# Kernel optimization log

Measured on AMD Instinct MI355X. Metric: run time of the kernel, lower is better.

The kernel has to match this reference:

```python
import jax, jax.numpy as jnp
import numpy as np

S, B, D, F, E, K = 1024, 2, 512, 2048, 8, 2


def setup_inputs() -> dict:
    key = jax.random.key(0)
    ks = jax.random.split(key, 12)
    s = lambda *sh: 1.0 / np.sqrt(sh[0])
    inp = {
        "x": jax.random.normal(ks[0], (S, B, D), dtype=jnp.float32),
        # gate: nn.Linear(d_model, n_experts)
        "Wg": jax.random.normal(ks[1], (D, E), dtype=jnp.float32) * s(D),
        "bg": jnp.zeros((E,), dtype=jnp.float32),
        # routed experts: stacked FFN params (E copies of expert)
        "W1": jax.random.normal(ks[2], (E, D, F), dtype=jnp.float32) * s(D),
        "b1": jnp.zeros((E, F), dtype=jnp.float32),
        "W2": jax.random.normal(ks[3], (E, F, D), dtype=jnp.float32) * s(F),
        "b2": jnp.zeros((E, D), dtype=jnp.float32),
        # shared expert (single FFN)
        "Ws1": jax.random.normal(ks[4], (D, F), dtype=jnp.float32) * s(D),
        "bs1": jnp.zeros((F,), dtype=jnp.float32),
        "Ws2": jax.random.normal(ks[5], (F, D), dtype=jnp.float32) * s(F),
        "bs2": jnp.zeros((D,), dtype=jnp.float32),
    }
    return inp


def reference(x, Wg, bg, W1, b1, W2, b2, Ws1, bs1, Ws2, bs2):
    # gate_logits: (S, B, E)
    gate_logits = jnp.einsum("sbd,de->sbe", x, Wg) + bg
    # top-k per token (eval mode: k = n_experts_per_token, t = 1.0)
    weights, selected = jax.lax.top_k(gate_logits, K)  # (S,B,K)
    weights = jax.nn.softmax(weights.astype(jnp.float32), axis=-1)
    # combine weights per expert: (S,B,E)
    onehot = jax.nn.one_hot(selected, E, dtype=weights.dtype)  # (S,B,K,E)
    comb = jnp.einsum("sbk,sbke->sbe", weights, onehot)
    # routed experts computed densely, combined with per-token routing weight
    h = jax.nn.relu(jnp.einsum("sbd,edf->sbef", x, W1) + b1)  # (S,B,E,F)
    y = jnp.einsum("sbef,efd->sbed", h, W2) + b2              # (S,B,E,D)
    out = jnp.einsum("sbe,sbed->sbd", comb, y)
    # shared expert, scaled by 1/k
    hs = jax.nn.relu(jnp.einsum("sbd,df->sbf", x, Ws1) + bs1)
    shared = jnp.einsum("sbf,fd->sbd", hs, Ws2) + bs2
    out = out + (1.0 / K) * shared
    return out
```

## Files before the change

kernel.cpp:

```cpp
#include <hip/hip_runtime.h>
#include <hip/hip_bf16.h>
#include <stdint.h>

#define TT 2048
#define DD 512
#define FF 2048
#define EE 8

typedef unsigned short u16;
typedef __attribute__((ext_vector_type(8))) unsigned short ushort8v;
typedef __attribute__((ext_vector_type(8))) short short8;
typedef __attribute__((ext_vector_type(4))) float float4v;

__device__ __forceinline__ u16 f2bf(float f) {
    unsigned u = __float_as_uint(f);
    u += 0x7FFF + ((u >> 16) & 1);
    return (u16)(u >> 16);
}

__device__ __forceinline__ void gl_lds16(const u16* g, u16* l) {
    __builtin_amdgcn_global_load_lds(
        (const __attribute__((address_space(1))) unsigned int*)g,
        (__attribute__((address_space(3))) unsigned int*)l, 16, 0, 0);
}

#define WS_HB   0ull
#define WS_XG   (WS_HB + 6144ull*2048*2)
#define WS_WT   (WS_XG + 2048ull*512*2)
#define WS_RTG  (WS_WT + 9ull*2048*512*2)
#define WS_ME   (WS_RTG + 64)
#define WS_MW   (WS_ME + 4096*4)
#define WS_RT   (WS_MW + 4096*4)
#define WS_WROW (WS_RT + 4096*4)

__global__ __launch_bounds__(256) void conv_k(const float* __restrict__ srcE,
                                              const float* __restrict__ srcS,
                                              u16* __restrict__ dst,
                                              int R, int C, int shC) {
    int mid = blockIdx.x >> 8;
    int t2  = blockIdx.x & 255;
    int tr = t2 >> shC, tc = t2 & ((1 << shC) - 1);
    int r0 = tr * 64, c0 = tc * 64;
    const float* src = (mid < 8) ? srcE + (size_t)mid * R * C : srcS;
    u16* dstm = dst + (size_t)mid * R * C;
    int t = threadIdx.x;
    __shared__ __align__(16) u16 Ls[64 * 72];
#pragma unroll
    for (int i = 0; i < 4; ++i) {
        int rr = (t >> 4) + i * 16;
        int cc = (t & 15) * 4;
        float4v v = *(const float4v*)(src + (size_t)(r0 + rr) * C + c0 + cc);
#pragma unroll
        for (int j = 0; j < 4; ++j) Ls[(cc + j) * 72 + rr] = f2bf(v[j]);
    }
    __syncthreads();
#pragma unroll
    for (int jj = 0; jj < 2; ++jj) {
        int slot = t + jj * 256;
        int cc = slot >> 3;
        int r8 = (slot & 7) * 8;
        ushort8v o = *(const ushort8v*)&Ls[cc * 72 + r8];
        *(ushort8v*)(dstm + (size_t)(c0 + cc) * R + r0 + r8) = o;
    }
}

__global__ void gate_k(const float* __restrict__ x, const float* __restrict__ Wg,
                       const float* __restrict__ bg,
                       int* __restrict__ metaE, float* __restrict__ metaW,
                       u16* __restrict__ xg) {
    int t = blockIdx.x;
    int lane = threadIdx.x;
    const float* xp = x + (size_t)t * DD + lane * 8;
    float4v x0 = *(const float4v*)xp;
    float4v x1 = *(const float4v*)(xp + 4);
    float xf[8] = {x0[0], x0[1], x0[2], x0[3], x1[0], x1[1], x1[2], x1[3]};
    float acc[EE] = {0.f, 0.f, 0.f, 0.f, 0.f, 0.f, 0.f, 0.f};
#pragma unroll
    for (int g = 0; g < 8; ++g) {
        int d = lane * 8 + g;
        const float* wp = Wg + (size_t)d * EE;
        float4v w0 = *(const float4v*)wp;
        float4v w1 = *(const float4v*)(wp + 4);
        acc[0] += xf[g] * w0[0]; acc[1] += xf[g] * w0[1];
        acc[2] += xf[g] * w0[2]; acc[3] += xf[g] * w0[3];
        acc[4] += xf[g] * w1[0]; acc[5] += xf[g] * w1[1];
        acc[6] += xf[g] * w1[2]; acc[7] += xf[g] * w1[3];
    }
#pragma unroll
    for (int off = 1; off < 64; off <<= 1) {
#pragma unroll
        for (int e = 0; e < EE; ++e) acc[e] += __shfl_xor(acc[e], off, 64);
    }
    ushort8v xv;
#pragma unroll
    for (int j = 0; j < 4; ++j) xv[j] = f2bf(x0[j]);
#pragma unroll
    for (int j = 0; j < 4; ++j) xv[4 + j] = f2bf(x1[j]);
    *(ushort8v*)(xg + (size_t)t * DD + lane * 8) = xv;
    if (lane == 0) {
#pragma unroll
        for (int e = 0; e < EE; ++e) acc[e] += bg[e];
        int e0 = 0; float l0 = acc[0];
#pragma unroll
        for (int e = 1; e < EE; ++e) if (acc[e] > l0) { l0 = acc[e]; e0 = e; }
        int e1 = -1; float l1 = -3.4e38f;
#pragma unroll
        for (int e = 0; e < EE; ++e)
            if (e != e0 && acc[e] > l1) { l1 = acc[e]; e1 = e; }
        float ex = __expf(l1 - l0);
        float w0 = 1.f / (1.f + ex);
        float w1 = 1.f - w0;
        metaE[2 * t] = e0; metaE[2 * t + 1] = e1;
        metaW[2 * t] = w0; metaW[2 * t + 1] = w1;
    }
}

__global__ __launch_bounds__(1024) void rank_k(const int* __restrict__ metaE,
                                               const float* __restrict__ metaW,
                                               int* __restrict__ routing,
                                               int* __restrict__ rtok,
                                               float* __restrict__ wrow) {
    int tid = threadIdx.x;
    int wv = tid >> 6, lane = tid & 63;
    __shared__ int segCnt[64][8];
    __shared__ int segBase[64][8];
    __shared__ int expOff[8];
    int myE[4], myRk[4];
    unsigned long long below = (lane == 0) ? 0ull : ((~0ull) >> (64 - lane));
#pragma unroll
    for (int r = 0; r < 4; ++r) {
        int entry = wv * 256 + r * 64 + lane;
        int e = metaE[entry];
        myE[r] = e;
        int rk = 0;
#pragma unroll
        for (int ee = 0; ee < 8; ++ee) {
            unsigned long long m = __ballot(e == ee);
            if (e == ee) rk = __popcll(m & below);
            if (lane == ee) segCnt[wv * 4 + r][ee] = __popcll(m);
        }
        myRk[r] = rk;
    }
    __syncthreads();
    if (tid < 8) {
        int s = 0;
        for (int g = 0; g < 64; ++g) { segBase[g][tid] = s; s += segCnt[g][tid]; }
        expOff[tid] = s;
    }
    __syncthreads();
    if (tid == 0) {
        int s = 0;
        for (int e = 0; e < 8; ++e) { int c = expOff[e]; expOff[e] = s; s += c; }
    }
    __syncthreads();
    if (tid < 8) {
        routing[tid] = expOff[tid];
        routing[8 + tid] = segBase[63][tid] + segCnt[63][tid];
    }
#pragma unroll
    for (int r = 0; r < 4; ++r) {
        int entry = wv * 256 + r * 64 + lane;
        int e = myE[r];
        int row = expOff[e] + segBase[wv * 4 + r][e] + myRk[r];
        rtok[row] = entry >> 1;
        wrow[row] = metaW[entry];
    }
}

__global__ __launch_bounds__(256) void gemmA_k(
    const u16* __restrict__ xg, const u16* __restrict__ Wt,
    const float* __restrict__ b1, const float* __restrict__ bs1,
    const int* __restrict__ routing, const int* __restrict__ rtok,
    u16* __restrict__ hbuf) {
    const int* offs = routing;
    const int* cnt = routing + 8;
    int vb = blockIdx.x;
    int tid = threadIdx.x;
    int rt, ct, Mloc, hRowBase, rowBase;
    bool routed;
    const u16* Bsrc;
    const float* bias;
    if (vb < 2048) {
        int e = vb & 7;
        int r2 = vb >> 3;
        rt = r2 >> 4; ct = r2 & 15;
        int M = cnt[e];
        if (rt * 128 >= M) return;
        Mloc = M - rt * 128;
        rowBase = offs[e] + rt * 128;
        Bsrc = Wt + (size_t)e * FF * DD;
        bias = b1 + e * FF;
        hRowBase = rowBase;
        routed = true;
    } else {
        int v = vb - 2048;
        rt = v >> 4; ct = v & 15;
        Mloc = 128;
        rowBase = rt * 128;
        Bsrc = Wt + (size_t)8 * FF * DD;
        bias = bs1;
        hRowBase = 4096 + rt * 128;
        routed = false;
    }
    int n0 = ct * 128;
    int lane = tid & 63, w = tid >> 6, ln = lane & 15, quad = lane >> 4;
    int rowL = lane >> 2;
    int kcL = (lane & 3) * 8;

    const u16* Abase[2];
#pragma unroll
    for (int i = 0; i < 2; ++i) {
        int seg = w * 2 + i;
        int rr = seg * 16 + rowL;
        int tok;
        if (routed) {
            int br = rowBase + rr;
            if (br > 4095) br = 4095;
            tok = rtok[br];
        } else {
            tok = rowBase + rr;
        }
        Abase[i] = xg + (size_t)tok * DD + kcL;
    }

    __shared__ __align__(16) u16 As[128 * 32];
    __shared__ __align__(16) u16 Bs[128 * 32];

    float4v acc[4][4];
#pragma unroll
    for (int a = 0; a < 4; ++a)
#pragma unroll
        for (int b = 0; b < 4; ++b) acc[a][b] = (float4v){0.f, 0.f, 0.f, 0.f};

    for (int kt = 0; kt < DD / 32; ++kt) {
        int k0 = kt * 32;
#pragma unroll
        for (int i = 0; i < 2; ++i) {
            int seg = w * 2 + i;
            int row = seg * 16 + rowL;
            gl_lds16(Abase[i] + k0, &As[seg * 512]);
            gl_lds16(Bsrc + (size_t)(n0 + row) * DD + k0 + kcL, &Bs[seg * 512]);
        }
        __syncthreads();
        short8 Af[4], Bf[4];
#pragma unroll
        for (int a = 0; a < 4; ++a)
            Af[a] = *(const short8*)&As[((w & 1) * 64 + a * 16 + ln) * 32 + quad * 8];
#pragma unroll
        for (int b = 0; b < 4; ++b)
            Bf[b] = *(const short8*)&Bs[((w >> 1) * 64 + b * 16 + ln) * 32 + quad * 8];
#pragma unroll
        for (int a = 0; a < 4; ++a)
#pragma unroll
            for (int b = 0; b < 4; ++b)
                acc[a][b] = __builtin_amdgcn_mfma_f32_16x16x32_bf16(Af[a], Bf[b], acc[a][b], 0, 0, 0);
        __syncthreads();
    }
#pragma unroll
    for (int b = 0; b < 4; ++b) {
        int n = n0 + (w >> 1) * 64 + b * 16 + ln;
        float bv = bias[n];
#pragma unroll
        for (int a = 0; a < 4; ++a) {
#pragma unroll
            for (int i = 0; i < 4; ++i) {
                int lr = (w & 1) * 64 + a * 16 + quad * 4 + i;
                if (lr < Mloc) {
                    float v = acc[a][b][i] + bv;
                    v = v > 0.f ? v : 0.f;
                    hbuf[(size_t)(hRowBase + lr) * FF + n] = f2bf(v);
                }
            }
        }
    }
}

__global__ __launch_bounds__(256) void gemmB_k(
    const u16* __restrict__ hbuf, const u16* __restrict__ Wt,
    const float* __restrict__ b2, const float* __restrict__ bs2,
    const int* __restrict__ routing, const int* __restrict__ rtok,
    const float* __restrict__ wrow, float* __restrict__ out) {
    const int* offs = routing;
    const int* cnt = routing + 8;
    int vb = blockIdx.x;
    int tid = threadIdx.x;
    int rt, ct, ks, Mloc, aRowBase;
    bool sh = vb >= 1024;
    const u16* Bsrc;
    const float* bias;
    if (!sh) {
        int e = vb & 7;
        int r2 = vb >> 3;
        rt = r2 >> 3; ct = (r2 >> 1) & 3; ks = r2 & 1;
        int M = cnt[e];
        if (rt * 128 >= M) return;
        Mloc = M - rt * 128;
        aRowBase = offs[e] + rt * 128;
        Bsrc = Wt + (size_t)e * DD * FF;
        bias = b2 + e * DD;
    } else {
        int v = vb - 1024;
        rt = v >> 3; ct = (v >> 1) & 3; ks = v & 1;
        Mloc = 128;
        aRowBase = 4096 + rt * 128;
        Bsrc = Wt + (size_t)8 * DD * FF;
        bias = bs2;
    }
    int n0 = ct * 128;
    int lane = tid & 63, w = tid >> 6, ln = lane & 15, quad = lane >> 4;
    int rowL = lane >> 2;
    int kcL = (lane & 3) * 8;

    __shared__ __align__(16) u16 As[128 * 32];
    __shared__ __align__(16) u16 Bs[128 * 32];

    float4v acc[4][4];
#pragma unroll
    for (int a = 0; a < 4; ++a)
#pragma unroll
        for (int b = 0; b < 4; ++b) acc[a][b] = (float4v){0.f, 0.f, 0.f, 0.f};

    const u16* Asrc = hbuf + (size_t)aRowBase * FF;

    for (int kt = 0; kt < 32; ++kt) {
        int k0 = ks * 1024 + kt * 32;
#pragma unroll
        for (int i = 0; i < 2; ++i) {
            int seg = w * 2 + i;
            int row = seg * 16 + rowL;
            gl_lds16(Asrc + (size_t)row * FF + k0 + kcL, &As[seg * 512]);
            gl_lds16(Bsrc + (size_t)(n0 + row) * FF + k0 + kcL, &Bs[seg * 512]);
        }
        __syncthreads();
        short8 Af[4], Bf[4];
#pragma unroll
        for (int a = 0; a < 4; ++a)
            Af[a] = *(const short8*)&As[((w & 1) * 64 + a * 16 + ln) * 32 + quad * 8];
#pragma unroll
        for (int b = 0; b < 4; ++b)
            Bf[b] = *(const short8*)&Bs[((w >> 1) * 64 + b * 16 + ln) * 32 + quad * 8];
#pragma unroll
        for (int a = 0; a < 4; ++a)
#pragma unroll
            for (int b = 0; b < 4; ++b)
                acc[a][b] = __builtin_amdgcn_mfma_f32_16x16x32_bf16(Af[a], Bf[b], acc[a][b], 0, 0, 0);
        __syncthreads();
    }
    float bv[4];
#pragma unroll
    for (int b = 0; b < 4; ++b)
        bv[b] = (ks == 0) ? bias[n0 + (w >> 1) * 64 + b * 16 + ln] : 0.f;
#pragma unroll
    for (int a = 0; a < 4; ++a) {
#pragma unroll
        for (int i = 0; i < 4; ++i) {
            int lr = (w & 1) * 64 + a * 16 + quad * 4 + i;
            if (lr < Mloc) {
                int row = aRowBase + lr;
                int t; float wr;
                if (sh) { t = row - 4096; wr = 0.5f; }
                else    { t = rtok[row];  wr = wrow[row]; }
                float* op = out + (size_t)t * DD;
#pragma unroll
                for (int b = 0; b < 4; ++b) {
                    int n = n0 + (w >> 1) * 64 + b * 16 + ln;
                    atomicAdd(op + n, wr * (acc[a][b][i] + bv[b]));
                }
            }
        }
    }
}

extern "C" void kernel_launch(void* const* d_in, const int* in_sizes, int n_in,
                              void* d_out, int out_size, void* d_ws, size_t ws_size,
                              hipStream_t stream) {
    const float* x   = (const float*)d_in[0];
    const float* Wg  = (const float*)d_in[1];
    const float* bg  = (const float*)d_in[2];
    const float* W1  = (const float*)d_in[3];
    const float* b1  = (const float*)d_in[4];
    const float* W2  = (const float*)d_in[5];
    const float* b2  = (const float*)d_in[6];
    const float* Ws1 = (const float*)d_in[7];
    const float* bs1 = (const float*)d_in[8];
    const float* Ws2 = (const float*)d_in[9];
    const float* bs2 = (const float*)d_in[10];
    float* out = (float*)d_out;

    char* ws = (char*)d_ws;
    u16*   hbuf    = (u16*)(ws + WS_HB);
    u16*   xg      = (u16*)(ws + WS_XG);
    u16*   Wt      = (u16*)(ws + WS_WT);
    int*   routing = (int*)(ws + WS_RTG);
    int*   metaE   = (int*)(ws + WS_ME);
    float* metaW   = (float*)(ws + WS_MW);
    int*   rtok    = (int*)(ws + WS_RT);
    float* wrow    = (float*)(ws + WS_WROW);

    hipMemsetAsync(d_out, 0, (size_t)out_size * sizeof(float), stream);

    conv_k<<<2304, 256, 0, stream>>>(W1, Ws1, Wt, DD, FF, 5);
    gate_k<<<TT, 64, 0, stream>>>(x, Wg, bg, metaE, metaW, xg);
    rank_k<<<1, 1024, 0, stream>>>(metaE, metaW, routing, rtok, wrow);
    gemmA_k<<<2304, 256, 0, stream>>>(xg, Wt, b1, bs1, routing, rtok, hbuf);
    conv_k<<<2304, 256, 0, stream>>>(W2, Ws2, Wt, FF, DD, 3);
    gemmB_k<<<1152, 256, 0, stream>>>(hbuf, Wt, b2, bs2, routing, rtok, wrow, out);
}
```

Measured before the change: 228.9 us.

## Fuse all MoE stages into one cooperative persistent kernel with grid syncs

Replaces the six separate launches plus memset with a single cooperative persistent kernel that loops over job lists, separated by grid-wide barriers. It also adds an XOR swizzle to LDS staging in both GEMMs to cut bank conflicts, raises gemmB's K-split from 2 to 4, and reorders jobs so shared-expert tiles come first. The aim is to remove launch gaps and tail effects. The cost is grid-sync overhead, a single-block rank phase that idles the rest of the GPU, and possible occupancy limits from the forced 4-blocks-per-SM bound.

```diff
diff --git a/kernel.cpp b/kernel.cpp
--- a/kernel.cpp
+++ b/kernel.cpp
@@ -1,11 +1,15 @@
 #include <hip/hip_runtime.h>
+#include <hip/hip_cooperative_groups.h>
 #include <hip/hip_bf16.h>
 #include <stdint.h>
+
+namespace cg = cooperative_groups;
 
 #define TT 2048
 #define DD 512
 #define FF 2048
 #define EE 8
+#define NJOB 2304
 
 typedef unsigned short u16;
 typedef __attribute__((ext_vector_type(8))) unsigned short ushort8v;
@@ -33,52 +37,50 @@
 #define WS_RT   (WS_MW + 4096*4)
 #define WS_WROW (WS_RT + 4096*4)
 
-__global__ __launch_bounds__(256) void conv_k(const float* __restrict__ srcE,
-                                              const float* __restrict__ srcS,
-                                              u16* __restrict__ dst,
-                                              int R, int C, int shC) {
-    int mid = blockIdx.x >> 8;
-    int t2  = blockIdx.x & 255;
+struct Params {
+    const float *x, *Wg, *bg, *W1, *b1, *W2, *b2, *Ws1, *bs1, *Ws2, *bs2;
+    float* out;
+    u16 *hbuf, *xg, *Wt;
+    int* routing; int* metaE; float* metaW; int* rtok; float* wrow;
+};
+
+__device__ void conv_unit(int j, const float* __restrict__ srcE,
+                          const float* __restrict__ srcS, u16* __restrict__ dst,
+                          int R, int C, int shC, u16* Ls) {
+    int mid = j >> 8, t2 = j & 255;
     int tr = t2 >> shC, tc = t2 & ((1 << shC) - 1);
     int r0 = tr * 64, c0 = tc * 64;
     const float* src = (mid < 8) ? srcE + (size_t)mid * R * C : srcS;
     u16* dstm = dst + (size_t)mid * R * C;
     int t = threadIdx.x;
-    __shared__ __align__(16) u16 Ls[64 * 72];
 #pragma unroll
     for (int i = 0; i < 4; ++i) {
         int rr = (t >> 4) + i * 16;
         int cc = (t & 15) * 4;
         float4v v = *(const float4v*)(src + (size_t)(r0 + rr) * C + c0 + cc);
 #pragma unroll
-        for (int j = 0; j < 4; ++j) Ls[(cc + j) * 72 + rr] = f2bf(v[j]);
+        for (int jx = 0; jx < 4; ++jx) Ls[(cc + jx) * 72 + rr] = f2bf(v[jx]);
     }
     __syncthreads();
 #pragma unroll
     for (int jj = 0; jj < 2; ++jj) {
         int slot = t + jj * 256;
-        int cc = slot >> 3;
-        int r8 = (slot & 7) * 8;
+        int cc = slot >> 3, r8 = (slot & 7) * 8;
         ushort8v o = *(const ushort8v*)&Ls[cc * 72 + r8];
         *(ushort8v*)(dstm + (size_t)(c0 + cc) * R + r0 + r8) = o;
     }
-}
-
-__global__ void gate_k(const float* __restrict__ x, const float* __restrict__ Wg,
-                       const float* __restrict__ bg,
-                       int* __restrict__ metaE, float* __restrict__ metaW,
-                       u16* __restrict__ xg) {
-    int t = blockIdx.x;
-    int lane = threadIdx.x;
-    const float* xp = x + (size_t)t * DD + lane * 8;
+    __syncthreads();
+}
+
+__device__ void gate_wave(int t, int lane, const Params& p) {
+    const float* xp = p.x + (size_t)t * DD + lane * 8;
     float4v x0 = *(const float4v*)xp;
     float4v x1 = *(const float4v*)(xp + 4);
     float xf[8] = {x0[0], x0[1], x0[2], x0[3], x1[0], x1[1], x1[2], x1[3]};
     float acc[EE] = {0.f, 0.f, 0.f, 0.f, 0.f, 0.f, 0.f, 0.f};
 #pragma unroll
     for (int g = 0; g < 8; ++g) {
-        int d = lane * 8 + g;
-        const float* wp = Wg + (size_t)d * EE;
+        const float* wp = p.Wg + (size_t)(lane * 8 + g) * EE;
         float4v w0 = *(const float4v*)wp;
         float4v w1 = *(const float4v*)(wp + 4);
         acc[0] += xf[g] * w0[0]; acc[1] += xf[g] * w0[1];
@@ -93,13 +95,13 @@
     }
     ushort8v xv;
 #pragma unroll
-    for (int j = 0; j < 4; ++j) xv[j] = f2bf(x0[j]);
-#pragma unroll
-    for (int j = 0; j < 4; ++j) xv[4 + j] = f2bf(x1[j]);
-    *(ushort8v*)(xg + (size_t)t * DD + lane * 8) = xv;
+    for (int jx = 0; jx < 4; ++jx) xv[jx] = f2bf(x0[jx]);
+#pragma unroll
+    for (int jx = 0; jx < 4; ++jx) xv[4 + jx] = f2bf(x1[jx]);
+    *(ushort8v*)(p.xg + (size_t)t * DD + lane * 8) = xv;
     if (lane == 0) {
 #pragma unroll
-        for (int e = 0; e < EE; ++e) acc[e] += bg[e];
+        for (int e = 0; e < EE; ++e) acc[e] += p.bg[e];
         int e0 = 0; float l0 = acc[0];
 #pragma unroll
         for (int e = 1; e < EE; ++e) if (acc[e] > l0) { l0 = acc[e]; e0 = e; }
@@ -109,129 +111,91 @@
             if (e != e0 && acc[e] > l1) { l1 = acc[e]; e1 = e; }
         float ex = __expf(l1 - l0);
         float w0 = 1.f / (1.f + ex);
-        float w1 = 1.f - w0;
-        metaE[2 * t] = e0; metaE[2 * t + 1] = e1;
-        metaW[2 * t] = w0; metaW[2 * t + 1] = w1;
-    }
-}
-
-__global__ __launch_bounds__(1024) void rank_k(const int* __restrict__ metaE,
-                                               const float* __restrict__ metaW,
-                                               int* __restrict__ routing,
-                                               int* __restrict__ rtok,
-                                               float* __restrict__ wrow) {
-    int tid = threadIdx.x;
-    int wv = tid >> 6, lane = tid & 63;
-    __shared__ int segCnt[64][8];
-    __shared__ int segBase[64][8];
-    __shared__ int expOff[8];
-    int myE[4], myRk[4];
+        p.metaE[2 * t] = e0; p.metaE[2 * t + 1] = e1;
+        p.metaW[2 * t] = w0; p.metaW[2 * t + 1] = 1.f - w0;
+    }
+}
+
+__device__ void rank_block(const Params& p, char* smem) {
+    u16* er      = (u16*)smem;
+    int* segCnt  = (int*)(smem + 8192);
+    int* segBase = (int*)(smem + 10240);
+    int* expTot  = (int*)(smem + 12288);
+    int tid = threadIdx.x, wv = tid >> 6, lane = tid & 63;
     unsigned long long below = (lane == 0) ? 0ull : ((~0ull) >> (64 - lane));
-#pragma unroll
-    for (int r = 0; r < 4; ++r) {
-        int entry = wv * 256 + r * 64 + lane;
-        int e = metaE[entry];
-        myE[r] = e;
+    for (int s = wv * 16; s < wv * 16 + 16; ++s) {
+        int entry = s * 64 + lane;
+        int e = p.metaE[entry];
         int rk = 0;
 #pragma unroll
         for (int ee = 0; ee < 8; ++ee) {
             unsigned long long m = __ballot(e == ee);
             if (e == ee) rk = __popcll(m & below);
-            if (lane == ee) segCnt[wv * 4 + r][ee] = __popcll(m);
-        }
-        myRk[r] = rk;
+            if (lane == ee) segCnt[s * 8 + ee] = __popcll(m);
+        }
+        er[entry] = (u16)(e | (rk << 4));
     }
     __syncthreads();
     if (tid < 8) {
         int s = 0;
-        for (int g = 0; g < 64; ++g) { segBase[g][tid] = s; s += segCnt[g][tid]; }
-        expOff[tid] = s;
+        for (int g = 0; g < 64; ++g) { segBase[g * 8 + tid] = s; s += segCnt[g * 8 + tid]; }
+        expTot[tid] = s;
     }
     __syncthreads();
     if (tid == 0) {
         int s = 0;
-        for (int e = 0; e < 8; ++e) { int c = expOff[e]; expOff[e] = s; s += c; }
-    }
-    __syncthreads();
-    if (tid < 8) {
-        routing[tid] = expOff[tid];
-        routing[8 + tid] = segBase[63][tid] + segCnt[63][tid];
-    }
-#pragma unroll
-    for (int r = 0; r < 4; ++r) {
-        int entry = wv * 256 + r * 64 + lane;
-        int e = myE[r];
-        int row = expOff[e] + segBase[wv * 4 + r][e] + myRk[r];
-        rtok[row] = entry >> 1;
-        wrow[row] = metaW[entry];
-    }
-}
-
-__global__ __launch_bounds__(256) void gemmA_k(
-    const u16* __restrict__ xg, const u16* __restrict__ Wt,
-    const float* __restrict__ b1, const float* __restrict__ bs1,
-    const int* __restrict__ routing, const int* __restrict__ rtok,
-    u16* __restrict__ hbuf) {
-    const int* offs = routing;
-    const int* cnt = routing + 8;
-    int vb = blockIdx.x;
+        for (int e = 0; e < 8; ++e) { int c = expTot[e]; expTot[8 + e] = s; s += c; }
+    }
+    __syncthreads();
+    if (tid < 8) { p.routing[tid] = expTot[8 + tid]; p.routing[8 + tid] = expTot[tid]; }
+    for (int i = 0; i < 16; ++i) {
+        int entry = tid + i * 256;
+        int v = er[entry];
+        int e = v & 15, rk = v >> 4;
+        int row = expTot[8 + e] + segBase[(entry >> 6) * 8 + e] + rk;
+        p.rtok[row] = entry >> 1;
+        p.wrow[row] = p.metaW[entry];
+    }
+    __syncthreads();
+}
+
+__device__ void gemmA_job(int j, const Params& p, u16* As, u16* Bs) {
+    const int* offs = p.routing; const int* cnt = p.routing + 8;
     int tid = threadIdx.x;
-    int rt, ct, Mloc, hRowBase, rowBase;
-    bool routed;
-    const u16* Bsrc;
-    const float* bias;
-    if (vb < 2048) {
-        int e = vb & 7;
-        int r2 = vb >> 3;
-        rt = r2 >> 4; ct = r2 & 15;
-        int M = cnt[e];
-        if (rt * 128 >= M) return;
-        Mloc = M - rt * 128;
-        rowBase = offs[e] + rt * 128;
-        Bsrc = Wt + (size_t)e * FF * DD;
-        bias = b1 + e * FF;
-        hRowBase = rowBase;
-        routed = true;
+    int rt, ct, Mloc, hRowBase, rowBase; bool routed;
+    const u16* Bsrc; const float* bias;
+    if (j < 256) {
+        rt = j >> 4; ct = j & 15; Mloc = 128; rowBase = rt * 128;
+        Bsrc = p.Wt + (size_t)8 * FF * DD; bias = p.bs1;
+        hRowBase = 4096 + rt * 128; routed = false;
     } else {
-        int v = vb - 2048;
-        rt = v >> 4; ct = v & 15;
-        Mloc = 128;
-        rowBase = rt * 128;
-        Bsrc = Wt + (size_t)8 * FF * DD;
-        bias = bs1;
-        hRowBase = 4096 + rt * 128;
-        routed = false;
+        int jr = j - 256; rt = jr >> 7; int rem = jr & 127;
+        int e = rem >> 4; ct = rem & 15;
+        int M = cnt[e]; if (rt * 128 >= M) return;
+        Mloc = M - rt * 128; rowBase = offs[e] + rt * 128;
+        Bsrc = p.Wt + (size_t)e * FF * DD; bias = p.b1 + e * FF;
+        hRowBase = rowBase; routed = true;
     }
     int n0 = ct * 128;
     int lane = tid & 63, w = tid >> 6, ln = lane & 15, quad = lane >> 4;
     int rowL = lane >> 2;
-    int kcL = (lane & 3) * 8;
-
+    int kS = ((lane & 3) ^ ((lane >> 3) & 3)) * 8;
     const u16* Abase[2];
 #pragma unroll
     for (int i = 0; i < 2; ++i) {
-        int seg = w * 2 + i;
-        int rr = seg * 16 + rowL;
+        int rr = (w * 2 + i) * 16 + rowL;
         int tok;
         if (routed) {
-            int br = rowBase + rr;
-            if (br > 4095) br = 4095;
-            tok = rtok[br];
-        } else {
-            tok = rowBase + rr;
-        }
-        Abase[i] = xg + (size_t)tok * DD + kcL;
-    }
-
-    __shared__ __align__(16) u16 As[128 * 32];
-    __shared__ __align__(16) u16 Bs[128 * 32];
-
+            int br = rowBase + rr; if (br > 4095) br = 4095;
+            tok = p.rtok[br];
+        } else tok = rowBase + rr;
+        Abase[i] = p.xg + (size_t)tok * DD + kS;
+    }
     float4v acc[4][4];
 #pragma unroll
     for (int a = 0; a < 4; ++a)
 #pragma unroll
         for (int b = 0; b < 4; ++b) acc[a][b] = (float4v){0.f, 0.f, 0.f, 0.f};
-
     for (int kt = 0; kt < DD / 32; ++kt) {
         int k0 = kt * 32;
 #pragma unroll
@@ -239,16 +203,17 @@
             int seg = w * 2 + i;
             int row = seg * 16 + rowL;
             gl_lds16(Abase[i] + k0, &As[seg * 512]);
-            gl_lds16(Bsrc + (size_t)(n0 + row) * DD + k0 + kcL, &Bs[seg * 512]);
+            gl_lds16(Bsrc + (size_t)(n0 + row) * DD + k0 + kS, &Bs[seg * 512]);
         }
         __syncthreads();
+        int rsw = (ln >> 1) & 3;
         short8 Af[4], Bf[4];
 #pragma unroll
         for (int a = 0; a < 4; ++a)
-            Af[a] = *(const short8*)&As[((w & 1) * 64 + a * 16 + ln) * 32 + quad * 8];
+            Af[a] = *(const short8*)&As[((w & 1) * 64 + a * 16 + ln) * 32 + ((quad ^ rsw) * 8)];
 #pragma unroll
         for (int b = 0; b < 4; ++b)
-            Bf[b] = *(const short8*)&Bs[((w >> 1) * 64 + b * 16 + ln) * 32 + quad * 8];
+            Bf[b] = *(const short8*)&Bs[((w >> 1) * 64 + b * 16 + ln) * 32 + ((quad ^ rsw) * 8)];
 #pragma unroll
         for (int a = 0; a < 4; ++a)
 #pragma unroll
@@ -268,77 +233,57 @@
                 if (lr < Mloc) {
                     float v = acc[a][b][i] + bv;
                     v = v > 0.f ? v : 0.f;
-                    hbuf[(size_t)(hRowBase + lr) * FF + n] = f2bf(v);
+                    p.hbuf[(size_t)(hRowBase + lr) * FF + n] = f2bf(v);
                 }
             }
         }
     }
 }
 
-__global__ __launch_bounds__(256) void gemmB_k(
-    const u16* __restrict__ hbuf, const u16* __restrict__ Wt,
-    const float* __restrict__ b2, const float* __restrict__ bs2,
-    const int* __restrict__ routing, const int* __restrict__ rtok,
-    const float* __restrict__ wrow, float* __restrict__ out) {
-    const int* offs = routing;
-    const int* cnt = routing + 8;
-    int vb = blockIdx.x;
+__device__ void gemmB_job(int j, const Params& p, u16* As, u16* Bs) {
+    const int* offs = p.routing; const int* cnt = p.routing + 8;
     int tid = threadIdx.x;
-    int rt, ct, ks, Mloc, aRowBase;
-    bool sh = vb >= 1024;
-    const u16* Bsrc;
-    const float* bias;
-    if (!sh) {
-        int e = vb & 7;
-        int r2 = vb >> 3;
-        rt = r2 >> 3; ct = (r2 >> 1) & 3; ks = r2 & 1;
-        int M = cnt[e];
-        if (rt * 128 >= M) return;
-        Mloc = M - rt * 128;
-        aRowBase = offs[e] + rt * 128;
-        Bsrc = Wt + (size_t)e * DD * FF;
-        bias = b2 + e * DD;
+    int rt, ct, ks, Mloc, aRowBase; bool sh;
+    const u16* Bsrc; const float* bias;
+    if (j < 256) {
+        sh = true; rt = j >> 4; int sub = j & 15; ct = sub >> 2; ks = sub & 3;
+        Mloc = 128; aRowBase = 4096 + rt * 128;
+        Bsrc = p.Wt + (size_t)8 * DD * FF; bias = p.bs2;
     } else {
-        int v = vb - 1024;
-        rt = v >> 3; ct = (v >> 1) & 3; ks = v & 1;
-        Mloc = 128;
-        aRowBase = 4096 + rt * 128;
-        Bsrc = Wt + (size_t)8 * DD * FF;
-        bias = bs2;
+        sh = false; int jr = j - 256; rt = jr >> 7; int rem = jr & 127;
+        int e = rem >> 4; int sub = rem & 15; ct = sub >> 2; ks = sub & 3;
+        int M = cnt[e]; if (rt * 128 >= M) return;
+        Mloc = M - rt * 128; aRowBase = offs[e] + rt * 128;
+        Bsrc = p.Wt + (size_t)e * DD * FF; bias = p.b2 + e * DD;
     }
     int n0 = ct * 128;
     int lane = tid & 63, w = tid >> 6, ln = lane & 15, quad = lane >> 4;
     int rowL = lane >> 2;
-    int kcL = (lane & 3) * 8;
-
-    __shared__ __align__(16) u16 As[128 * 32];
-    __shared__ __align__(16) u16 Bs[128 * 32];
-
+    int kS = ((lane & 3) ^ ((lane >> 3) & 3)) * 8;
+    const u16* Asrc = p.hbuf + (size_t)aRowBase * FF;
     float4v acc[4][4];
 #pragma unroll
     for (int a = 0; a < 4; ++a)
 #pragma unroll
         for (int b = 0; b < 4; ++b) acc[a][b] = (float4v){0.f, 0.f, 0.f, 0.f};
-
-    const u16* Asrc = hbuf + (size_t)aRowBase * FF;
-
-    for (int kt = 0; kt < 32; ++kt) {
-        int k0 = ks * 1024 + kt * 32;
+    for (int kt = 0; kt < 16; ++kt) {
+        int k0 = ks * 512 + kt * 32;
 #pragma unroll
         for (int i = 0; i < 2; ++i) {
             int seg = w * 2 + i;
             int row = seg * 16 + rowL;
-            gl_lds16(Asrc + (size_t)row * FF + k0 + kcL, &As[seg * 512]);
-            gl_lds16(Bsrc + (size_t)(n0 + row) * FF + k0 + kcL, &Bs[seg * 512]);
+            gl_lds16(Asrc + (size_t)row * FF + k0 + kS, &As[seg * 512]);
+            gl_lds16(Bsrc + (size_t)(n0 + row) * FF + k0 + kS, &Bs[seg * 512]);
         }
         __syncthreads();
+        int rsw = (ln >> 1) & 3;
         short8 Af[4], Bf[4];
 #pragma unroll
         for (int a = 0; a < 4; ++a)
-            Af[a] = *(const short8*)&As[((w & 1) * 64 + a * 16 + ln) * 32 + quad * 8];
+            Af[a] = *(const short8*)&As[((w & 1) * 64 + a * 16 + ln) * 32 + ((quad ^ rsw) * 8)];
 #pragma unroll
         for (int b = 0; b < 4; ++b)
-            Bf[b] = *(const short8*)&Bs[((w >> 1) * 64 + b * 16 + ln) * 32 + quad * 8];
+            Bf[b] = *(const short8*)&Bs[((w >> 1) * 64 + b * 16 + ln) * 32 + ((quad ^ rsw) * 8)];
 #pragma unroll
         for (int a = 0; a < 4; ++a)
 #pragma unroll
@@ -359,8 +304,8 @@
                 int row = aRowBase + lr;
                 int t; float wr;
                 if (sh) { t = row - 4096; wr = 0.5f; }
-                else    { t = rtok[row];  wr = wrow[row]; }
-                float* op = out + (size_t)t * DD;
+                else    { t = p.rtok[row]; wr = p.wrow[row]; }
+                float* op = p.out + (size_t)t * DD;
 #pragma unroll
                 for (int b = 0; b < 4; ++b) {
                     int n = n0 + (w >> 1) * 64 + b * 16 + ln;
@@ -371,38 +316,62 @@
     }
 }
 
+__global__ __launch_bounds__(256, 4) void mega_k(Params p) {
+    __shared__ __align__(16) char smem[16384];
+    u16* As = (u16*)smem;
+    u16* Bs = (u16*)(smem + 8192);
+    u16* Ls = (u16*)smem;
+    cg::grid_group grid = cg::this_grid();
+    int b = blockIdx.x, tid = threadIdx.x, G = gridDim.x;
+
+    for (size_t i = (size_t)b * 256 + tid; i * 4 < (size_t)TT * DD; i += (size_t)G * 256)
+        *(float4v*)(p.out + i * 4) = (float4v){0.f, 0.f, 0.f, 0.f};
+    for (int j = b; j < NJOB; j += G) conv_unit(j, p.W1, p.Ws1, p.Wt, DD, FF, 5, Ls);
+    {
+        int wid = b * 4 + (tid >> 6), lane = tid & 63;
+        for (int t = wid; t < TT; t += G * 4) gate_wave(t, lane, p);
+    }
+    grid.sync();
+    if (b == 0) rank_block(p, smem);
+    grid.sync();
+    for (int j = b; j < NJOB; j += G) gemmA_job(j, p, As, Bs);
+    grid.sync();
+    for (int j = b; j < NJOB; j += G) conv_unit(j, p.W2, p.Ws2, p.Wt, FF, DD, 3, Ls);
+    grid.sync();
+    for (int j = b; j < NJOB; j += G) gemmB_job(j, p, As, Bs);
+}
+
 extern "C" void kernel_launch(void* const* d_in, const int* in_sizes, int n_in,
                               void* d_out, int out_size, void* d_ws, size_t ws_size,
                               hipStream_t stream) {
-    const float* x   = (const float*)d_in[0];
-    const float* Wg  = (const float*)d_in[1];
-    const float* bg  = (const float*)d_in[2];
-    const float* W1  = (const float*)d_in[3];
-    const float* b1  = (const float*)d_in[4];
-    const float* W2  = (const float*)d_in[5];
-    const float* b2  = (const float*)d_in[6];
-    const float* Ws1 = (const float*)d_in[7];
-    const float* bs1 = (const float*)d_in[8];
-    const float* Ws2 = (const float*)d_in[9];
-    const float* bs2 = (const float*)d_in[10];
-    float* out = (float*)d_out;
-
     char* ws = (char*)d_ws;
-    u16*   hbuf    = (u16*)(ws + WS_HB);
-    u16*   xg      = (u16*)(ws + WS_XG);
-    u16*   Wt      = (u16*)(ws + WS_WT);
-    int*   routing = (int*)(ws + WS_RTG);
-    int*   metaE   = (int*)(ws + WS_ME);
-    float* metaW   = (float*)(ws + WS_MW);
-    int*   rtok    = (int*)(ws + WS_RT);
-    float* wrow    = (float*)(ws + WS_WROW);
-
-    hipMemsetAsync(d_out, 0, (size_t)out_size * sizeof(float), stream);
-
-    conv_k<<<2304, 256, 0, stream>>>(W1, Ws1, Wt, DD, FF, 5);
-    gate_k<<<TT, 64, 0, stream>>>(x, Wg, bg, metaE, metaW, xg);
-    rank_k<<<1, 1024, 0, stream>>>(metaE, metaW, routing, rtok, wrow);
-    gemmA_k<<<2304, 256, 0, stream>>>(xg, Wt, b1, bs1, routing, rtok, hbuf);
-    conv_k<<<2304, 256, 0, stream>>>(W2, Ws2, Wt, FF, DD, 3);
-    gemmB_k<<<1152, 256, 0, stream>>>(hbuf, Wt, b2, bs2, routing, rtok, wrow, out);
-}
+    Params p;
+    p.x   = (const float*)d_in[0];
+    p.Wg  = (const float*)d_in[1];
+    p.bg  = (const float*)d_in[2];
+    p.W1  = (const float*)d_in[3];
+    p.b1  = (const float*)d_in[4];
+    p.W2  = (const float*)d_in[5];
+    p.b2  = (const float*)d_in[6];
+    p.Ws1 = (const float*)d_in[7];
+    p.bs1 = (const float*)d_in[8];
+    p.Ws2 = (const float*)d_in[9];
+    p.bs2 = (const float*)d_in[10];
+    p.out = (float*)d_out;
+    p.hbuf    = (u16*)(ws + WS_HB);
+    p.xg      = (u16*)(ws + WS_XG);
+    p.Wt      = (u16*)(ws + WS_WT);
+    p.routing = (int*)(ws + WS_RTG);
+    p.metaE   = (int*)(ws + WS_ME);
+    p.metaW   = (float*)(ws + WS_MW);
+    p.rtok    = (int*)(ws + WS_RT);
+    p.wrow    = (float*)(ws + WS_WROW);
+
+    int maxB = 0;
+    hipOccupancyMaxActiveBlocksPerMultiprocessor(&maxB, mega_k, 256, 0);
+    if (maxB < 1) maxB = 1;
+    if (maxB > 4) maxB = 4;
+    dim3 gridD(256 * maxB), blockD(256);
+    void* kp[] = { (void*)&p };
+    hipLaunchCooperativeKernel((void*)mega_k, gridD, blockD, kp, 0, stream);
+}
```

Result: slower. 519.2 us (+126.8%).

## Fuse weight conversion, gating and output zeroing; swizzle LDS; split-K four ways

Applied to the files above, without the earlier changes.

Merges the W1/W2 bf16 transpose-conversion, gate/top-k and output zeroing into one launch, replacing the memset and several separate kernels. When the workspace is large enough, W2 is converted up front into its own buffer. Both GEMMs now use an XOR swizzle on the LDS k-chunk to avoid bank conflicts. The block order is changed so shared-expert tiles come first, and gemmB splits K four ways instead of two, which doubles its blocks and its atomic adds. The extra workspace and atomic traffic may offset the saved launches.

```diff
diff --git a/kernel.cpp b/kernel.cpp
--- a/kernel.cpp
+++ b/kernel.cpp
@@ -26,50 +26,50 @@
 
 #define WS_HB   0ull
 #define WS_XG   (WS_HB + 6144ull*2048*2)
-#define WS_WT   (WS_XG + 2048ull*512*2)
-#define WS_RTG  (WS_WT + 9ull*2048*512*2)
+#define WS_WT1  (WS_XG + 2048ull*512*2)
+#define WS_RTG  (WS_WT1 + 9ull*2048*512*2)
 #define WS_ME   (WS_RTG + 64)
 #define WS_MW   (WS_ME + 4096*4)
 #define WS_RT   (WS_MW + 4096*4)
 #define WS_WROW (WS_RT + 4096*4)
-
-__global__ __launch_bounds__(256) void conv_k(const float* __restrict__ srcE,
-                                              const float* __restrict__ srcS,
-                                              u16* __restrict__ dst,
-                                              int R, int C, int shC) {
-    int mid = blockIdx.x >> 8;
-    int t2  = blockIdx.x & 255;
+#define WS_WT2  (WS_WROW + 4096*4)
+#define WS_NEED (WS_WT2 + 9ull*2048*512*2)
+
+__device__ __forceinline__ void conv_unit(int j, const float* __restrict__ srcE,
+                                          const float* __restrict__ srcS,
+                                          u16* __restrict__ dst,
+                                          int R, int C, int shC, u16* Ls) {
+    int mid = j >> 8, t2 = j & 255;
     int tr = t2 >> shC, tc = t2 & ((1 << shC) - 1);
     int r0 = tr * 64, c0 = tc * 64;
     const float* src = (mid < 8) ? srcE + (size_t)mid * R * C : srcS;
     u16* dstm = dst + (size_t)mid * R * C;
     int t = threadIdx.x;
-    __shared__ __align__(16) u16 Ls[64 * 72];
 #pragma unroll
     for (int i = 0; i < 4; ++i) {
         int rr = (t >> 4) + i * 16;
         int cc = (t & 15) * 4;
         float4v v = *(const float4v*)(src + (size_t)(r0 + rr) * C + c0 + cc);
 #pragma unroll
-        for (int j = 0; j < 4; ++j) Ls[(cc + j) * 72 + rr] = f2bf(v[j]);
+        for (int jx = 0; jx < 4; ++jx) Ls[(cc + jx) * 72 + rr] = f2bf(v[jx]);
     }
     __syncthreads();
 #pragma unroll
     for (int jj = 0; jj < 2; ++jj) {
         int slot = t + jj * 256;
-        int cc = slot >> 3;
-        int r8 = (slot & 7) * 8;
+        int cc = slot >> 3, r8 = (slot & 7) * 8;
         ushort8v o = *(const ushort8v*)&Ls[cc * 72 + r8];
         *(ushort8v*)(dstm + (size_t)(c0 + cc) * R + r0 + r8) = o;
     }
 }
 
-__global__ void gate_k(const float* __restrict__ x, const float* __restrict__ Wg,
-                       const float* __restrict__ bg,
-                       int* __restrict__ metaE, float* __restrict__ metaW,
-                       u16* __restrict__ xg) {
-    int t = blockIdx.x;
-    int lane = threadIdx.x;
+__device__ __forceinline__ void gate_wave(int t, int lane,
+                                          const float* __restrict__ x,
+                                          const float* __restrict__ Wg,
+                                          const float* __restrict__ bg,
+                                          int* __restrict__ metaE,
+                                          float* __restrict__ metaW,
+                                          u16* __restrict__ xg) {
     const float* xp = x + (size_t)t * DD + lane * 8;
     float4v x0 = *(const float4v*)xp;
     float4v x1 = *(const float4v*)(xp + 4);
@@ -77,8 +77,7 @@
     float acc[EE] = {0.f, 0.f, 0.f, 0.f, 0.f, 0.f, 0.f, 0.f};
 #pragma unroll
     for (int g = 0; g < 8; ++g) {
-        int d = lane * 8 + g;
-        const float* wp = Wg + (size_t)d * EE;
+        const float* wp = Wg + (size_t)(lane * 8 + g) * EE;
         float4v w0 = *(const float4v*)wp;
         float4v w1 = *(const float4v*)(wp + 4);
         acc[0] += xf[g] * w0[0]; acc[1] += xf[g] * w0[1];
@@ -93,9 +92,9 @@
     }
     ushort8v xv;
 #pragma unroll
-    for (int j = 0; j < 4; ++j) xv[j] = f2bf(x0[j]);
-#pragma unroll
-    for (int j = 0; j < 4; ++j) xv[4 + j] = f2bf(x1[j]);
+    for (int jx = 0; jx < 4; ++jx) xv[jx] = f2bf(x0[jx]);
+#pragma unroll
+    for (int jx = 0; jx < 4; ++jx) xv[4 + jx] = f2bf(x1[jx]);
     *(ushort8v*)(xg + (size_t)t * DD + lane * 8) = xv;
     if (lane == 0) {
 #pragma unroll
@@ -109,10 +108,42 @@
             if (e != e0 && acc[e] > l1) { l1 = acc[e]; e1 = e; }
         float ex = __expf(l1 - l0);
         float w0 = 1.f / (1.f + ex);
-        float w1 = 1.f - w0;
         metaE[2 * t] = e0; metaE[2 * t + 1] = e1;
-        metaW[2 * t] = w0; metaW[2 * t + 1] = w1;
-    }
+        metaW[2 * t] = w0; metaW[2 * t + 1] = 1.f - w0;
+    }
+}
+
+__global__ __launch_bounds__(256) void fused1_k(
+    const float* __restrict__ x, const float* __restrict__ Wg,
+    const float* __restrict__ bg,
+    const float* __restrict__ W1, const float* __restrict__ Ws1,
+    const float* __restrict__ W2, const float* __restrict__ Ws2,
+    float* __restrict__ out, u16* __restrict__ xg,
+    u16* __restrict__ Wt1, u16* __restrict__ Wt2,
+    int* __restrict__ metaE, float* __restrict__ metaW, int nconv) {
+    __shared__ __align__(16) u16 Ls[64 * 72];
+    int b = blockIdx.x, tid = threadIdx.x;
+    if (b < nconv) {
+        if (b < 2304) conv_unit(b, W1, Ws1, Wt1, DD, FF, 5, Ls);
+        else          conv_unit(b - 2304, W2, Ws2, Wt2, FF, DD, 3, Ls);
+    } else if (b < nconv + 512) {
+        int gb = b - nconv;
+        int t = gb * 4 + (tid >> 6);
+        gate_wave(t, tid & 63, x, Wg, bg, metaE, metaW, xg);
+    } else {
+        int zb = b - nconv - 512;
+        float* op = out + (size_t)zb * 8192;
+#pragma unroll
+        for (int it = 0; it < 8; ++it)
+            *(float4v*)(op + it * 1024 + tid * 4) = (float4v){0.f, 0.f, 0.f, 0.f};
+    }
+}
+
+__global__ __launch_bounds__(256) void conv2_k(const float* __restrict__ W2,
+                                               const float* __restrict__ Ws2,
+                                               u16* __restrict__ Wt2) {
+    __shared__ __align__(16) u16 Ls[64 * 72];
+    conv_unit(blockIdx.x, W2, Ws2, Wt2, FF, DD, 3, Ls);
 }
 
 __global__ __launch_bounds__(1024) void rank_k(const int* __restrict__ metaE,
@@ -172,66 +203,44 @@
     const float* __restrict__ b1, const float* __restrict__ bs1,
     const int* __restrict__ routing, const int* __restrict__ rtok,
     u16* __restrict__ hbuf) {
-    const int* offs = routing;
-    const int* cnt = routing + 8;
-    int vb = blockIdx.x;
-    int tid = threadIdx.x;
-    int rt, ct, Mloc, hRowBase, rowBase;
-    bool routed;
-    const u16* Bsrc;
-    const float* bias;
-    if (vb < 2048) {
-        int e = vb & 7;
-        int r2 = vb >> 3;
-        rt = r2 >> 4; ct = r2 & 15;
-        int M = cnt[e];
-        if (rt * 128 >= M) return;
-        Mloc = M - rt * 128;
-        rowBase = offs[e] + rt * 128;
-        Bsrc = Wt + (size_t)e * FF * DD;
-        bias = b1 + e * FF;
-        hRowBase = rowBase;
-        routed = true;
+    const int* offs = routing; const int* cnt = routing + 8;
+    int j = blockIdx.x, tid = threadIdx.x;
+    int rt, ct, Mloc, hRowBase, rowBase; bool routed;
+    const u16* Bsrc; const float* bias;
+    if (j < 256) {
+        rt = j >> 4; ct = j & 15; Mloc = 128; rowBase = rt * 128;
+        Bsrc = Wt + (size_t)8 * FF * DD; bias = bs1;
+        hRowBase = 4096 + rt * 128; routed = false;
     } else {
-        int v = vb - 2048;
-        rt = v >> 4; ct = v & 15;
-        Mloc = 128;
-        rowBase = rt * 128;
-        Bsrc = Wt + (size_t)8 * FF * DD;
-        bias = bs1;
-        hRowBase = 4096 + rt * 128;
-        routed = false;
+        int jr = j - 256; rt = jr >> 7; int rem = jr & 127;
+        int e = rem >> 4; ct = rem & 15;
+        int M = cnt[e]; if (rt * 128 >= M) return;
+        Mloc = M - rt * 128; rowBase = offs[e] + rt * 128;
+        Bsrc = Wt + (size_t)e * FF * DD; bias = b1 + e * FF;
+        hRowBase = rowBase; routed = true;
     }
     int n0 = ct * 128;
     int lane = tid & 63, w = tid >> 6, ln = lane & 15, quad = lane >> 4;
     int rowL = lane >> 2;
-    int kcL = (lane & 3) * 8;
-
+    int kS = ((lane & 3) ^ ((lane >> 3) & 3)) * 8;
     const u16* Abase[2];
 #pragma unroll
     for (int i = 0; i < 2; ++i) {
-        int seg = w * 2 + i;
-        int rr = seg * 16 + rowL;
+        int rr = (w * 2 + i) * 16 + rowL;
         int tok;
         if (routed) {
-            int br = rowBase + rr;
-            if (br > 4095) br = 4095;
+            int br = rowBase + rr; if (br > 4095) br = 4095;
             tok = rtok[br];
-        } else {
-            tok = rowBase + rr;
-        }
-        Abase[i] = xg + (size_t)tok * DD + kcL;
-    }
-
+        } else tok = rowBase + rr;
+        Abase[i] = xg + (size_t)tok * DD + kS;
+    }
     __shared__ __align__(16) u16 As[128 * 32];
     __shared__ __align__(16) u16 Bs[128 * 32];
-
     float4v acc[4][4];
 #pragma unroll
     for (int a = 0; a < 4; ++a)
 #pragma unroll
         for (int b = 0; b < 4; ++b) acc[a][b] = (float4v){0.f, 0.f, 0.f, 0.f};
-
     for (int kt = 0; kt < DD / 32; ++kt) {
         int k0 = kt * 32;
 #pragma unroll
@@ -239,16 +248,17 @@
             int seg = w * 2 + i;
             int row = seg * 16 + rowL;
             gl_lds16(Abase[i] + k0, &As[seg * 512]);
-            gl_lds16(Bsrc + (size_t)(n0 + row) * DD + k0 + kcL, &Bs[seg * 512]);
+            gl_lds16(Bsrc + (size_t)(n0 + row) * DD + k0 + kS, &Bs[seg * 512]);
         }
         __syncthreads();
+        int rsw = (ln >> 1) & 3;
         short8 Af[4], Bf[4];
 #pragma unroll
         for (int a = 0; a < 4; ++a)
-            Af[a] = *(const short8*)&As[((w & 1) * 64 + a * 16 + ln) * 32 + quad * 8];
+            Af[a] = *(const short8*)&As[((w & 1) * 64 + a * 16 + ln) * 32 + ((quad ^ rsw) * 8)];
 #pragma unroll
         for (int b = 0; b < 4; ++b)
-            Bf[b] = *(const short8*)&Bs[((w >> 1) * 64 + b * 16 + ln) * 32 + quad * 8];
+            Bf[b] = *(const short8*)&Bs[((w >> 1) * 64 + b * 16 + ln) * 32 + ((quad ^ rsw) * 8)];
 #pragma unroll
         for (int a = 0; a < 4; ++a)
 #pragma unroll
@@ -280,65 +290,51 @@
     const float* __restrict__ b2, const float* __restrict__ bs2,
     const int* __restrict__ routing, const int* __restrict__ rtok,
     const float* __restrict__ wrow, float* __restrict__ out) {
-    const int* offs = routing;
-    const int* cnt = routing + 8;
-    int vb = blockIdx.x;
-    int tid = threadIdx.x;
-    int rt, ct, ks, Mloc, aRowBase;
-    bool sh = vb >= 1024;
-    const u16* Bsrc;
-    const float* bias;
-    if (!sh) {
-        int e = vb & 7;
-        int r2 = vb >> 3;
-        rt = r2 >> 3; ct = (r2 >> 1) & 3; ks = r2 & 1;
-        int M = cnt[e];
-        if (rt * 128 >= M) return;
-        Mloc = M - rt * 128;
-        aRowBase = offs[e] + rt * 128;
-        Bsrc = Wt + (size_t)e * DD * FF;
-        bias = b2 + e * DD;
+    const int* offs = routing; const int* cnt = routing + 8;
+    int j = blockIdx.x, tid = threadIdx.x;
+    int rt, ct, ks, Mloc, aRowBase; bool sh;
+    const u16* Bsrc; const float* bias;
+    if (j < 256) {
+        sh = true; rt = j >> 4; int sub = j & 15; ct = sub >> 2; ks = sub & 3;
+        Mloc = 128; aRowBase = 4096 + rt * 128;
+        Bsrc = Wt + (size_t)8 * DD * FF; bias = bs2;
     } else {
-        int v = vb - 1024;
-        rt = v >> 3; ct = (v >> 1) & 3; ks = v & 1;
-        Mloc = 128;
-        aRowBase = 4096 + rt * 128;
-        Bsrc = Wt + (size_t)8 * DD * FF;
-        bias = bs2;
+        sh = false; int jr = j - 256; rt = jr >> 7; int rem = jr & 127;
+        int e = rem >> 4; int sub = rem & 15; ct = sub >> 2; ks = sub & 3;
+        int M = cnt[e]; if (rt * 128 >= M) return;
+        Mloc = M - rt * 128; aRowBase = offs[e] + rt * 128;
+        Bsrc = Wt + (size_t)e * DD * FF; bias = b2 + e * DD;
     }
     int n0 = ct * 128;
     int lane = tid & 63, w = tid >> 6, ln = lane & 15, quad = lane >> 4;
     int rowL = lane >> 2;
-    int kcL = (lane & 3) * 8;
-
+    int kS = ((lane & 3) ^ ((lane >> 3) & 3)) * 8;
+    const u16* Asrc = hbuf + (size_t)aRowBase * FF;
     __shared__ __align__(16) u16 As[128 * 32];
     __shared__ __align__(16) u16 Bs[128 * 32];
-
     float4v acc[4][4];
 #pragma unroll
     for (int a = 0; a < 4; ++a)
 #pragma unroll
         for (int b = 0; b < 4; ++b) acc[a][b] = (float4v){0.f, 0.f, 0.f, 0.f};
-
-    const u16* Asrc = hbuf + (size_t)aRowBase * FF;
-
-    for (int kt = 0; kt < 32; ++kt) {
-        int k0 = ks * 1024 + kt * 32;
+    for (int kt = 0; kt < 16; ++kt) {
+        int k0 = ks * 512 + kt * 32;
 #pragma unroll
         for (int i = 0; i < 2; ++i) {
             int seg = w * 2 + i;
             int row = seg * 16 + rowL;
-            gl_lds16(Asrc + (size_t)row * FF + k0 + kcL, &As[seg * 512]);
-            gl_lds16(Bsrc + (size_t)(n0 + row) * FF + k0 + kcL, &Bs[seg * 512]);
+            gl_lds16(Asrc + (size_t)row * FF + k0 + kS, &As[seg * 512]);
+            gl_lds16(Bsrc + (size_t)(n0 + row) * FF + k0 + kS, &Bs[seg * 512]);
         }
         __syncthreads();
+        int rsw = (ln >> 1) & 3;
         short8 Af[4], Bf[4];
 #pragma unroll
         for (int a = 0; a < 4; ++a)
-            Af[a] = *(const short8*)&As[((w & 1) * 64 + a * 16 + ln) * 32 + quad * 8];
+            Af[a] = *(const short8*)&As[((w & 1) * 64 + a * 16 + ln) * 32 + ((quad ^ rsw) * 8)];
 #pragma unroll
         for (int b = 0; b < 4; ++b)
-            Bf[b] = *(const short8*)&Bs[((w >> 1) * 64 + b * 16 + ln) * 32 + quad * 8];
+            Bf[b] = *(const short8*)&Bs[((w >> 1) * 64 + b * 16 + ln) * 32 + ((quad ^ rsw) * 8)];
 #pragma unroll
         for (int a = 0; a < 4; ++a)
 #pragma unroll
@@ -359,7 +355,7 @@
                 int row = aRowBase + lr;
                 int t; float wr;
                 if (sh) { t = row - 4096; wr = 0.5f; }
-                else    { t = rtok[row];  wr = wrow[row]; }
+                else    { t = rtok[row]; wr = wrow[row]; }
                 float* op = out + (size_t)t * DD;
 #pragma unroll
                 for (int b = 0; b < 4; ++b) {
@@ -390,19 +386,21 @@
     char* ws = (char*)d_ws;
     u16*   hbuf    = (u16*)(ws + WS_HB);
     u16*   xg      = (u16*)(ws + WS_XG);
-    u16*   Wt      = (u16*)(ws + WS_WT);
+    u16*   Wt1     = (u16*)(ws + WS_WT1);
     int*   routing = (int*)(ws + WS_RTG);
     int*   metaE   = (int*)(ws + WS_ME);
     float* metaW   = (float*)(ws + WS_MW);
     int*   rtok    = (int*)(ws + WS_RT);
     float* wrow    = (float*)(ws + WS_WROW);
 
-    hipMemsetAsync(d_out, 0, (size_t)out_size * sizeof(float), stream);
-
-    conv_k<<<2304, 256, 0, stream>>>(W1, Ws1, Wt, DD, FF, 5);
-    gate_k<<<TT, 64, 0, stream>>>(x, Wg, bg, metaE, metaW, xg);
+    bool big = ws_size >= WS_NEED;
+    u16* Wt2 = big ? (u16*)(ws + WS_WT2) : Wt1;
+    int nconv = big ? 4608 : 2304;
+
+    fused1_k<<<nconv + 640, 256, 0, stream>>>(x, Wg, bg, W1, Ws1, W2, Ws2,
+                                              out, xg, Wt1, Wt2, metaE, metaW, nconv);
     rank_k<<<1, 1024, 0, stream>>>(metaE, metaW, routing, rtok, wrow);
-    gemmA_k<<<2304, 256, 0, stream>>>(xg, Wt, b1, bs1, routing, rtok, hbuf);
-    conv_k<<<2304, 256, 0, stream>>>(W2, Ws2, Wt, FF, DD, 3);
-    gemmB_k<<<1152, 256, 0, stream>>>(hbuf, Wt, b2, bs2, routing, rtok, wrow, out);
-}
+    gemmA_k<<<2304, 256, 0, stream>>>(xg, Wt1, b1, bs1, routing, rtok, hbuf);
+    if (!big) conv2_k<<<2304, 256, 0, stream>>>(W2, Ws2, Wt2);
+    gemmB_k<<<2304, 256, 0, stream>>>(hbuf, Wt2, b2, bs2, routing, rtok, wrow, out);
+}
```

Measured after the change: 246.5 us. 1.08x slower.
